# Optimization experiments

Hardware: AMD Instinct MI355X
Metric: run time of the kernel (lower is better)

Reference implementation:

```python
import jax, jax.numpy as jnp
import numpy as np

N = 50000      # nodes
E = 600000     # edges
DIN = 128      # dim_in
DOUT = 128     # dim_out (mulhead=1)
DG = 64        # dim_gate


def setup_inputs() -> dict:
    key = jax.random.key(0)
    ks = jax.random.split(key, 10)
    rows = jax.random.randint(ks[0], (E,), 0, N, dtype=jnp.int32)   # dest nodes
    cols = jax.random.randint(ks[1], (E,), 0, N, dtype=jnp.int32)   # src nodes
    vals = jax.random.uniform(ks[2], (E,), dtype=jnp.float32)       # adj_norm values
    feat = jax.random.normal(ks[3], (N, DIN), dtype=jnp.float32)
    s = 1.0 / np.sqrt(DIN)
    W0 = jax.random.normal(ks[4], (DIN, DOUT), dtype=jnp.float32) * s
    b0 = jnp.zeros((DOUT,), dtype=jnp.float32)
    W1 = jax.random.normal(ks[5], (DIN, DOUT), dtype=jnp.float32) * s
    b1 = jnp.zeros((DOUT,), dtype=jnp.float32)
    att = jax.random.normal(ks[6], (2 * DOUT,), dtype=jnp.float32) * 0.1  # attention param [1, 2*DOUT] flattened
    W_pool = jax.random.normal(ks[7], (DIN, DG), dtype=jnp.float32) * s    # weight_pool_gate
    W_gate = jax.random.normal(ks[8], (2 * DIN + DG, 1), dtype=jnp.float32) * 0.05  # weight_gate, mulhead=1
    offset0 = jnp.zeros((DOUT,), dtype=jnp.float32)
    scale0 = jnp.ones((DOUT,), dtype=jnp.float32)
    offset1 = jnp.zeros((DOUT,), dtype=jnp.float32)
    scale1 = jnp.ones((DOUT,), dtype=jnp.float32)
    return dict(rows=rows, cols=cols, vals=vals, feat=feat, W0=W0, b0=b0,
                W1=W1, b1=b1, att=att, W_pool=W_pool, W_gate=W_gate,
                offset0=offset0, scale0=scale0, offset1=offset1, scale1=scale1)


def _batch_norm(x, scale, offset):
    # per-node norm over the feature dim (unbiased=False), matching _batch_norm
    m = x.mean(axis=1, keepdims=True)
    v = x.var(axis=1, keepdims=True) + 1e-9
    return (x - m) * scale * jax.lax.rsqrt(v) + offset


def reference(rows, cols, vals, feat, W0, b0, W1, b1, att, W_pool, W_gate,
              offset0, scale0, offset1, scale1):
    n = feat.shape[0]
    d = W0.shape[1]
    # --- gate value (GaAN eq. 3) ---
    zj = feat @ W_pool                                   # [N, DG]
    neigh_zj = jax.ops.segment_max(zj[cols], rows, num_segments=n)  # per-row max over neighbors
    neigh_zj = jnp.where(jnp.isfinite(neigh_zj), neigh_zj, 0.0)     # empty rows -> zeros
    neigh_mean = jax.ops.segment_sum(vals[:, None] * feat[cols], rows, num_segments=n)  # spmm(adj, feat)
    gate = jnp.concatenate([feat, neigh_zj, neigh_mean], axis=1) @ W_gate  # [N, 1]
    # --- per-order feature transforms (order=1, mulhead=1) ---
    h0 = jax.nn.relu(feat @ W0 + b0)                     # order 0 (self)
    h1 = jax.nn.relu(feat @ W1 + b1)                     # order 1 (neighbor)
    # --- sparse attention aggregation ---
    a_self = jax.nn.leaky_relu(h0 @ att[:d], 0.2)        # [N]
    a_neigh = jax.nn.leaky_relu(h1 @ att[d:], 0.2)       # [N]
    e = a_self[rows] + a_neigh[cols]                     # per-edge score (replaces adj values)
    agg = jax.ops.segment_sum(e[:, None] * h1[cols], rows, num_segments=n)  # spmm(att_adj, h1)
    agg = agg * gate[:, :1]                              # gated
    # --- per-node batch norm, then 'mean' aggregation (sum of orders) ---
    return _batch_norm(h0, scale0, offset0) + _batch_norm(agg, scale1, offset1)
```

## Files before the change

kernel.cpp:

```cpp
#include <hip/hip_runtime.h>

#define DIN 128
#define DG 64

static __device__ __forceinline__ unsigned short f2bf(float x) {
    unsigned u = __builtin_bit_cast(unsigned, x);
    u = (u + 0x7FFF + ((u >> 16) & 1)) >> 16;
    return (unsigned short)u;
}
static __device__ __forceinline__ float bf2f(unsigned short s) {
    return __builtin_bit_cast(float, (unsigned)s << 16);
}

__global__ void k_deg(const int* __restrict__ rows, int* __restrict__ deg,
                      int* __restrict__ slot, int E) {
    int e = blockIdx.x * blockDim.x + threadIdx.x;
    if (e < E) slot[e] = atomicAdd(&deg[rows[e]], 1);
}

__global__ __launch_bounds__(1024) void k_scan1(const int* __restrict__ deg,
                                                int* __restrict__ rowptr,
                                                int* __restrict__ bsum, int n) {
    __shared__ int wsum[16];
    __shared__ int woff[16];
    int tid = threadIdx.x;
    int lane = tid & 63, w = tid >> 6;
    int i = blockIdx.x * 1024 + tid;
    int v = (i < n) ? deg[i] : 0;
    int x = v;
    #pragma unroll
    for (int off = 1; off < 64; off <<= 1) {
        int y = __shfl_up(x, off, 64);
        if (lane >= off) x += y;
    }
    if (lane == 63) wsum[w] = x;
    __syncthreads();
    if (w == 0) {
        int t = (lane < 16) ? wsum[lane] : 0;
        int xx = t;
        #pragma unroll
        for (int off = 1; off < 16; off <<= 1) {
            int y = __shfl_up(xx, off, 64);
            if (lane >= off) xx += y;
        }
        if (lane < 16) woff[lane] = xx - t;
    }
    __syncthreads();
    if (i < n) rowptr[i] = x - v + woff[w];
    if (tid == 1023) bsum[blockIdx.x] = woff[15] + wsum[15];
}

__global__ void k_scan2(const int* __restrict__ bsum, int* __restrict__ boff,
                        int* __restrict__ rowptr, int nb, int n) {
    int lane = threadIdx.x;
    int v = (lane < nb) ? bsum[lane] : 0;
    int x = v;
    #pragma unroll
    for (int off = 1; off < 64; off <<= 1) {
        int y = __shfl_up(x, off, 64);
        if (lane >= off) x += y;
    }
    boff[lane] = x - v;
    if (lane == 63) rowptr[n] = x;
}

__global__ void k_scan3(int* __restrict__ rowptr, const int* __restrict__ boff, int n) {
    int i = blockIdx.x * blockDim.x + threadIdx.x;
    if (i < n) rowptr[i] += boff[i >> 10];
}

__global__ void k_scatter(const int* __restrict__ rows, const int* __restrict__ cols,
                          const float* __restrict__ vals,
                          const int* __restrict__ rowptr, const int* __restrict__ slot,
                          int2* __restrict__ cv, int E) {
    int e = blockIdx.x * blockDim.x + threadIdx.x;
    if (e < E) {
        int dst = rowptr[rows[e]] + slot[e];
        cv[dst] = make_int2(cols[e], __builtin_bit_cast(int, vals[e]));
    }
}

__global__ void k_edgemeta(const int2* __restrict__ cv,
                           const float* __restrict__ a_neigh,
                           const float* __restrict__ fdotg,
                           float4* __restrict__ meta, int E) {
    int j = blockIdx.x * blockDim.x + threadIdx.x;
    if (j < E) {
        int2 p = cv[j];
        int c = p.x;
        float val = __builtin_bit_cast(float, p.y);
        meta[j] = make_float4(__builtin_bit_cast(float, c),
                              a_neigh[c], val * fdotg[c], 0.f);
    }
}

#define AS_LD 132
template<int TN, int TTN, int MODE>
static __device__ __forceinline__ void gemm_body(
    const float* __restrict__ feat, const float* __restrict__ B,
    const float* __restrict__ bias,
    const float* __restrict__ att, const float* __restrict__ Wg,
    float* __restrict__ h0, unsigned short* __restrict__ hb, float* __restrict__ zj,
    float* __restrict__ a_self, float* __restrict__ a_neigh,
    float* __restrict__ gpart, float* __restrict__ fdotg,
    int N, float* As, float* Bs) {
    int tid = threadIdx.x;
    int tx = tid & 15, ty = tid >> 4;
    int m0 = blockIdx.x * 128;
    float acc[8][TTN];
    #pragma unroll
    for (int r = 0; r < 8; ++r)
        #pragma unroll
        for (int c = 0; c < TTN; ++c) acc[r][c] = 0.f;
    float gdot[8], fdot[8];
    #pragma unroll
    for (int r = 0; r < 8; ++r) { gdot[r] = 0.f; fdot[r] = 0.f; }

    for (int kc = 0; kc < 128; kc += 32) {
        for (int i = tid; i < 1024; i += 256) {
            int m = i >> 3, kq = (i & 7) << 2;
            int node = m0 + m;
            float4 f;
            if (node < N) f = *(const float4*)&feat[(size_t)node * 128 + kc + kq];
            else          f = make_float4(0.f, 0.f, 0.f, 0.f);
            As[(kq + 0) * AS_LD + m] = f.x;
            As[(kq + 1) * AS_LD + m] = f.y;
            As[(kq + 2) * AS_LD + m] = f.z;
            As[(kq + 3) * AS_LD + m] = f.w;
        }
        for (int i = tid; i < 8 * TN; i += 256) {
            int k = i / (TN / 4), cq = (i % (TN / 4)) << 2;
            *(float4*)&Bs[k * TN + cq] = *(const float4*)&B[(size_t)(kc + k) * TN + cq];
        }
        __syncthreads();
        #pragma unroll 8
        for (int kk = 0; kk < 32; ++kk) {
            const float* ar = &As[kk * AS_LD];
            float4 a0 = *(const float4*)(ar + 4 * tx);
            float4 a1 = *(const float4*)(ar + 64 + 4 * tx);
            const float* br = &Bs[kk * TN + TTN * ty];
            float4 b0v = *(const float4*)br;
            float a[8] = {a0.x, a0.y, a0.z, a0.w, a1.x, a1.y, a1.z, a1.w};
            float b[TTN];
            b[0] = b0v.x; b[1] = b0v.y; b[2] = b0v.z; b[3] = b0v.w;
            if (TTN == 8) {
                float4 b1v = *(const float4*)(br + 4);
                b[4] = b1v.x; b[5] = b1v.y; b[6] = b1v.z; b[7] = b1v.w;
            }
            #pragma unroll
            for (int r = 0; r < 8; ++r)
                #pragma unroll
                for (int c = 0; c < TTN; ++c) acc[r][c] += a[r] * b[c];
            if (MODE == 0) {
                float g1 = Wg[kc + kk];
                float g2 = Wg[192 + kc + kk];
                #pragma unroll
                for (int r = 0; r < 8; ++r) {
                    gdot[r] += a[r] * g1;
                    fdot[r] += a[r] * g2;
                }
            }
        }
        __syncthreads();
    }
    float bb[TTN];
    #pragma unroll
    for (int c = 0; c < TTN; ++c) bb[c] = (MODE == 2) ? 0.f : bias[TTN * ty + c];
    float attv[TTN];
    if (MODE <= 1) {
        #pragma unroll
        for (int c = 0; c < TTN; ++c) attv[c] = att[(MODE == 0 ? 0 : 128) + TTN * ty + c];
    }
    float* red = Bs;
    #pragma unroll
    for (int r = 0; r < 8; ++r) {
        int ridx = (r < 4) ? (4 * tx + r) : (64 + 4 * tx + (r - 4));
        int node = m0 + ridx;
        float v[TTN];
        #pragma unroll
        for (int c = 0; c < TTN; ++c) {
            v[c] = acc[r][c] + bb[c];
            if (MODE != 2) v[c] = fmaxf(v[c], 0.f);
        }
        if (MODE <= 1) {
            float pa = 0.f;
            #pragma unroll
            for (int c = 0; c < TTN; ++c) pa += v[c] * attv[c];
            red[ty * 128 + ridx] = pa;
        }
        if (node < N) {
            if (MODE == 0) {
                #pragma unroll
                for (int g = 0; g < TTN / 4; ++g)
                    *(float4*)&h0[(size_t)node * 128 + TTN * ty + g * 4] =
                        make_float4(v[g*4], v[g*4+1], v[g*4+2], v[g*4+3]);
            } else if (MODE == 1) {
                unsigned p[4];
                #pragma unroll
                for (int g = 0; g < 4; ++g)
                    p[g] = (unsigned)f2bf(v[2*g]) | ((unsigned)f2bf(v[2*g+1]) << 16);
                *(uint4*)&hb[(size_t)node * 128 + 8 * ty] = make_uint4(p[0], p[1], p[2], p[3]);
            } else {
                *(float4*)&zj[(size_t)node * 64 + 4 * ty] =
                    make_float4(v[0], v[1], v[2], v[3]);
            }
        }
    }
    if (MODE == 0 && ty == 0) {
        #pragma unroll
        for (int r = 0; r < 8; ++r) {
            int ridx = (r < 4) ? (4 * tx + r) : (64 + 4 * tx + (r - 4));
            int node = m0 + ridx;
            if (node < N) { gpart[node] = gdot[r]; fdotg[node] = fdot[r]; }
        }
    }
    if (MODE <= 1) {
        __syncthreads();
        if (tid < 128) {
            float s = 0.f;
            #pragma unroll
            for (int t = 0; t < 16; ++t) s += red[t * 128 + tid];
            int node = m0 + tid;
            if (node < N) {
                float av = (s >= 0.f) ? s : 0.2f * s;
                if (MODE == 0) a_self[node] = av;
                else           a_neigh[node] = av;
            }
        }
    }
}

__global__ __launch_bounds__(256) void k_gemm3(
    const float* __restrict__ feat,
    const float* __restrict__ W0, const float* __restrict__ b0,
    const float* __restrict__ W1, const float* __restrict__ b1,
    const float* __restrict__ Wp,
    const float* __restrict__ att, const float* __restrict__ Wg,
    float* __restrict__ h0, unsigned short* __restrict__ hb, float* __restrict__ zj,
    float* __restrict__ a_self, float* __restrict__ a_neigh,
    float* __restrict__ gpart, float* __restrict__ fdotg, int N) {
    __shared__ float As[32 * AS_LD];
    __shared__ float Bs[32 * 128];
    int g = blockIdx.y;
    if (g == 0)      gemm_body<128, 8, 0>(feat, W0, b0, att, Wg, h0, hb, zj, a_self, a_neigh, gpart, fdotg, N, As, Bs);
    else if (g == 1) gemm_body<128, 8, 1>(feat, W1, b1, att, Wg, h0, hb, zj, a_self, a_neigh, gpart, fdotg, N, As, Bs);
    else             gemm_body< 64, 4, 2>(feat, Wp, nullptr, att, Wg, h0, hb, zj, a_self, a_neigh, gpart, fdotg, N, As, Bs);
}

template<int C>
static __device__ __forceinline__ void agg_chunk(
    const float4* __restrict__ meta, int j, int lane, float asr,
    const unsigned short* __restrict__ hb, const float* __restrict__ zj,
    float2& acca, float& zmax, float& vfsum) {
    float4 m[C];
    #pragma unroll
    for (int t = 0; t < C; ++t) m[t] = meta[j + t];
    ushort2 hv[C]; float zv[C];
    #pragma unroll
    for (int t = 0; t < C; ++t) {
        int c = __builtin_bit_cast(int, m[t].x);
        hv[t] = ((const ushort2*)(hb + (size_t)c * 128))[lane];
        zv[t] = zj[(size_t)c * 64 + lane];
    }
    #pragma unroll
    for (int t = 0; t < C; ++t) {
        float es = asr + m[t].y;
        acca.x += es * bf2f(hv[t].x);
        acca.y += es * bf2f(hv[t].y);
        zmax = fmaxf(zmax, zv[t]);
        vfsum += m[t].z;
    }
}

__global__ __launch_bounds__(256) void k_aggregate(
    const float4* __restrict__ meta, const int* __restrict__ rowptr,
    const float* __restrict__ h0, const unsigned short* __restrict__ hb,
    const float* __restrict__ zj,
    const float* __restrict__ a_self, const float* __restrict__ gpart,
    const float* __restrict__ Wg,
    const float* __restrict__ scale0, const float* __restrict__ offset0,
    const float* __restrict__ scale1, const float* __restrict__ offset1,
    float* __restrict__ out, int N) {
    int r = blockIdx.x * 4 + (threadIdx.x >> 6);
    int lane = threadIdx.x & 63;
    if (r >= N) return;
    int jb = rowptr[r], je = rowptr[r + 1];
    float2 acca = {0.f, 0.f};
    float zmax = -__builtin_inff();
    float vfsum = 0.f;
    float asr = a_self[r];
    int j = jb;
    while (j + 8 <= je) { agg_chunk<8>(meta, j, lane, asr, hb, zj, acca, zmax, vfsum); j += 8; }
    if (j + 4 <= je)    { agg_chunk<4>(meta, j, lane, asr, hb, zj, acca, zmax, vfsum); j += 4; }
    while (j < je)      { agg_chunk<1>(meta, j, lane, asr, hb, zj, acca, zmax, vfsum); j += 1; }
    if (jb == je) zmax = 0.f;
    float gs = zmax * Wg[128 + lane];
    #pragma unroll
    for (int off = 32; off; off >>= 1) gs += __shfl_xor(gs, off, 64);
    float gate = gpart[r] + gs + vfsum;
    float2 ag = {acca.x * gate, acca.y * gate};
    float2 x0 = ((const float2*)(h0 + (size_t)r * 128))[lane];
    float m0s = x0.x + x0.y;
    #pragma unroll
    for (int off = 32; off; off >>= 1) m0s += __shfl_xor(m0s, off, 64);
    float m0 = m0s * (1.f / 128.f);
    float d0x = x0.x - m0, d0y = x0.y - m0;
    float v0s = d0x * d0x + d0y * d0y;
    #pragma unroll
    for (int off = 32; off; off >>= 1) v0s += __shfl_xor(v0s, off, 64);
    float inv0 = rsqrtf(v0s * (1.f / 128.f) + 1e-9f);
    float m1s = ag.x + ag.y;
    #pragma unroll
    for (int off = 32; off; off >>= 1) m1s += __shfl_xor(m1s, off, 64);
    float m1 = m1s * (1.f / 128.f);
    float d1x = ag.x - m1, d1y = ag.y - m1;
    float v1s = d1x * d1x + d1y * d1y;
    #pragma unroll
    for (int off = 32; off; off >>= 1) v1s += __shfl_xor(v1s, off, 64);
    float inv1 = rsqrtf(v1s * (1.f / 128.f) + 1e-9f);
    float2 sc0 = ((const float2*)scale0)[lane], of0 = ((const float2*)offset0)[lane];
    float2 sc1 = ((const float2*)scale1)[lane], of1 = ((const float2*)offset1)[lane];
    float2 o;
    o.x = d0x * sc0.x * inv0 + of0.x + d1x * sc1.x * inv1 + of1.x;
    o.y = d0y * sc0.y * inv0 + of0.y + d1y * sc1.y * inv1 + of1.y;
    ((float2*)(out + (size_t)r * 128))[lane] = o;
}

extern "C" void kernel_launch(void* const* d_in, const int* in_sizes, int n_in,
                              void* d_out, int out_size, void* d_ws, size_t ws_size,
                              hipStream_t stream) {
    const int*   rows   = (const int*)d_in[0];
    const int*   cols   = (const int*)d_in[1];
    const float* vals   = (const float*)d_in[2];
    const float* feat   = (const float*)d_in[3];
    const float* W0     = (const float*)d_in[4];
    const float* b0     = (const float*)d_in[5];
    const float* W1     = (const float*)d_in[6];
    const float* b1     = (const float*)d_in[7];
    const float* att    = (const float*)d_in[8];
    const float* Wp     = (const float*)d_in[9];
    const float* Wg     = (const float*)d_in[10];
    const float* offset0 = (const float*)d_in[11];
    const float* scale0  = (const float*)d_in[12];
    const float* offset1 = (const float*)d_in[13];
    const float* scale1  = (const float*)d_in[14];
    float* out = (float*)d_out;

    const int E = in_sizes[0];
    const int N = in_sizes[3] / DIN;

    char* ws = (char*)d_ws;
    float* h0          = (float*)ws;          ws += (size_t)N * 128 * sizeof(float);
    unsigned short* hb = (unsigned short*)ws; ws += (size_t)N * 128 * sizeof(unsigned short);
    float* zj          = (float*)ws;          ws += (size_t)N * 64 * sizeof(float);
    float* a_self  = (float*)ws; ws += (size_t)N * sizeof(float);
    float* a_neigh = (float*)ws; ws += (size_t)N * sizeof(float);
    float* gpart   = (float*)ws; ws += (size_t)N * sizeof(float);
    float* fdotg   = (float*)ws; ws += (size_t)N * sizeof(float);
    int* deg      = (int*)ws; ws += (size_t)(N + 1) * sizeof(int);
    int* rowptr   = (int*)ws; ws += (size_t)(N + 1) * sizeof(int);
    int* bsum     = (int*)ws; ws += 64 * sizeof(int);
    int* boff     = (int*)ws; ws += 64 * sizeof(int);
    int* slot     = (int*)ws; ws += (size_t)E * sizeof(int);
    int2* cv      = (int2*)ws; ws += (size_t)E * sizeof(int2);
    ws = (char*)(((size_t)ws + 15) & ~(size_t)15);
    float4* meta  = (float4*)ws; ws += (size_t)E * sizeof(float4);

    hipMemsetAsync(deg, 0, (size_t)(N + 1) * sizeof(int), stream);

    k_deg<<<(E + 255) / 256, 256, 0, stream>>>(rows, deg, slot, E);
    int nb = (N + 1023) >> 10;
    k_scan1<<<nb, 1024, 0, stream>>>(deg, rowptr, bsum, N);
    k_scan2<<<1, 64, 0, stream>>>(bsum, boff, rowptr, nb, N);
    k_scan3<<<(N + 255) / 256, 256, 0, stream>>>(rowptr, boff, N);
    k_scatter<<<(E + 255) / 256, 256, 0, stream>>>(rows, cols, vals, rowptr, slot, cv, E);

    int mt = (N + 127) / 128;
    dim3 gg(mt, 3);
    k_gemm3<<<gg, 256, 0, stream>>>(feat, W0, b0, W1, b1, Wp, att, Wg,
                                    h0, hb, zj, a_self, a_neigh, gpart, fdotg, N);

    k_edgemeta<<<(E + 255) / 256, 256, 0, stream>>>(cv, a_neigh, fdotg, meta, E);

    int nb4 = (N + 3) / 4;
    k_aggregate<<<nb4, 256, 0, stream>>>(meta, rowptr, h0, hb, zj,
                                         a_self, gpart, Wg,
                                         scale0, offset0, scale1, offset1, out, N);
}
```

Baseline: 278.2 us.

## Move W0/W1 GEMMs to bf16 MFMA and fuse scatter with edge metadata

Replaces the fp32 FMA GEMM for the W0 and W1 transforms with a bf16 MFMA kernel. A new prep kernel converts feat to bf16 and computes the gate dot products, and a tiny kernel transposes the weights into bf16. The Wpool GEMM stays fp32 in its own kernel. The separate scatter and edge-metadata passes are merged into one kernel that writes meta directly, which drops the cv intermediate array. This cuts GEMM compute time and one pass over the edges, at the cost of bf16 precision in h0 and extra launches plus a feat conversion pass.

Result: no change. 280.8 us (+1.0%).

```diff
diff --git a/kernel.cpp b/kernel.cpp
--- a/kernel.cpp
+++ b/kernel.cpp
@@ -2,6 +2,9 @@
 
 #define DIN 128
 #define DG 64
+
+typedef __attribute__((ext_vector_type(8))) short short8;
+typedef __attribute__((ext_vector_type(4))) float f32x4;
 
 static __device__ __forceinline__ unsigned short f2bf(float x) {
     unsigned u = __builtin_bit_cast(unsigned, x);
@@ -69,53 +72,143 @@
     if (i < n) rowptr[i] += boff[i >> 10];
 }
 
-__global__ void k_scatter(const int* __restrict__ rows, const int* __restrict__ cols,
-                          const float* __restrict__ vals,
-                          const int* __restrict__ rowptr, const int* __restrict__ slot,
-                          int2* __restrict__ cv, int E) {
-    int e = blockIdx.x * blockDim.x + threadIdx.x;
-    if (e < E) {
-        int dst = rowptr[rows[e]] + slot[e];
-        cv[dst] = make_int2(cols[e], __builtin_bit_cast(int, vals[e]));
-    }
-}
-
-__global__ void k_edgemeta(const int2* __restrict__ cv,
-                           const float* __restrict__ a_neigh,
-                           const float* __restrict__ fdotg,
-                           float4* __restrict__ meta, int E) {
-    int j = blockIdx.x * blockDim.x + threadIdx.x;
-    if (j < E) {
-        int2 p = cv[j];
-        int c = p.x;
-        float val = __builtin_bit_cast(float, p.y);
-        meta[j] = make_float4(__builtin_bit_cast(float, c),
-                              a_neigh[c], val * fdotg[c], 0.f);
+__global__ __launch_bounds__(256) void k_prep(
+    const float* __restrict__ feat, const float* __restrict__ Wg,
+    unsigned short* __restrict__ featb,
+    float* __restrict__ gpart, float* __restrict__ fdotg, int N, int Npad) {
+    int r = blockIdx.x * 4 + (threadIdx.x >> 6);
+    int lane = threadIdx.x & 63;
+    if (r >= Npad) return;
+    if (r >= N) {
+        ((ushort2*)(featb + (size_t)r * 128))[lane] = make_ushort2(0, 0);
+        return;
+    }
+    float2 f = ((const float2*)(feat + (size_t)r * 128))[lane];
+    ((ushort2*)(featb + (size_t)r * 128))[lane] = make_ushort2(f2bf(f.x), f2bf(f.y));
+    float2 G  = ((const float2*)Wg)[lane];
+    float2 G2 = ((const float2*)(Wg + 192))[lane];
+    float s2 = f.x * G.x + f.y * G.y;
+    float s3 = f.x * G2.x + f.y * G2.y;
+    #pragma unroll
+    for (int off = 32; off; off >>= 1) {
+        s2 += __shfl_xor(s2, off, 64);
+        s3 += __shfl_xor(s3, off, 64);
+    }
+    if (lane == 0) { gpart[r] = s2; fdotg[r] = s3; }
+}
+
+__global__ __launch_bounds__(256) void k_wt(
+    const float* __restrict__ W0, const float* __restrict__ W1,
+    unsigned short* __restrict__ Bt) {
+    int c = threadIdx.x;
+    const float* W = (c < 128) ? W0 : W1;
+    int cc = c & 127;
+    for (int k = 0; k < 128; ++k)
+        Bt[c * 128 + k] = f2bf(W[k * 128 + cc]);
+}
+
+#define ALD 136
+__global__ __launch_bounds__(256) void k_gemm_mfma(
+    const unsigned short* __restrict__ featb, const unsigned short* __restrict__ Bt,
+    const float* __restrict__ b0, const float* __restrict__ b1,
+    const float* __restrict__ att,
+    float* __restrict__ h0, unsigned short* __restrict__ hb,
+    float* __restrict__ a_self, float* __restrict__ a_neigh, int N) {
+    __shared__ unsigned short As[64 * ALD];
+    __shared__ float sredA[128], nredA[128];
+    int tid = threadIdx.x;
+    int m0 = blockIdx.x * 64;
+    for (int i = tid; i < 1024; i += 256) {
+        int row = i >> 4, ch = i & 15;
+        uint4 v = *(const uint4*)&featb[(size_t)(m0 + row) * 128 + ch * 8];
+        *(uint4*)&As[row * ALD + ch * 8] = v;
+    }
+    __syncthreads();
+    int w = tid >> 6, lane = tid & 63;
+    int lm = lane & 15, q = lane >> 4;
+    f32x4 acc[4][4];
+    #pragma unroll
+    for (int rt = 0; rt < 4; ++rt)
+        #pragma unroll
+        for (int ct = 0; ct < 4; ++ct)
+            #pragma unroll
+            for (int r = 0; r < 4; ++r) acc[rt][ct][r] = 0.f;
+    #pragma unroll
+    for (int ks = 0; ks < 4; ++ks) {
+        short8 a[4], b[4];
+        #pragma unroll
+        for (int rt = 0; rt < 4; ++rt)
+            a[rt] = *(const short8*)&As[(rt * 16 + lm) * ALD + ks * 32 + q * 8];
+        #pragma unroll
+        for (int ct = 0; ct < 4; ++ct)
+            b[ct] = *(const short8*)&Bt[(size_t)(w * 64 + ct * 16 + lm) * 128 + ks * 32 + q * 8];
+        #pragma unroll
+        for (int rt = 0; rt < 4; ++rt)
+            #pragma unroll
+            for (int ct = 0; ct < 4; ++ct)
+                acc[rt][ct] = __builtin_amdgcn_mfma_f32_16x16x32_bf16(a[rt], b[ct], acc[rt][ct], 0, 0, 0);
+    }
+    float sacc[4][4];
+    #pragma unroll
+    for (int rt = 0; rt < 4; ++rt)
+        #pragma unroll
+        for (int r = 0; r < 4; ++r) sacc[rt][r] = 0.f;
+    #pragma unroll
+    for (int ct = 0; ct < 4; ++ct) {
+        int col = w * 64 + ct * 16 + lm;
+        float attc = att[col];
+        float bias = (w < 2) ? b0[col] : b1[col - 128];
+        #pragma unroll
+        for (int rt = 0; rt < 4; ++rt) {
+            #pragma unroll
+            for (int r = 0; r < 4; ++r) {
+                float v = acc[rt][ct][r] + bias;
+                v = fmaxf(v, 0.f);
+                sacc[rt][r] += v * attc;
+                int node = m0 + rt * 16 + q * 4 + r;
+                if (node < N) {
+                    if (w < 2) h0[(size_t)node * 128 + col] = v;
+                    else       hb[(size_t)node * 128 + (col - 128)] = f2bf(v);
+                }
+            }
+        }
+    }
+    float* red = (w < 2) ? sredA : nredA;
+    #pragma unroll
+    for (int rt = 0; rt < 4; ++rt)
+        #pragma unroll
+        for (int r = 0; r < 4; ++r) {
+            float s = sacc[rt][r];
+            s += __shfl_xor(s, 1, 64); s += __shfl_xor(s, 2, 64);
+            s += __shfl_xor(s, 4, 64); s += __shfl_xor(s, 8, 64);
+            if (lm == 0) red[(w & 1) * 64 + rt * 16 + q * 4 + r] = s;
+        }
+    __syncthreads();
+    if (tid < 64) {
+        int node = m0 + tid;
+        if (node < N) {
+            float s  = sredA[tid] + sredA[64 + tid];
+            float nn = nredA[tid] + nredA[64 + tid];
+            a_self[node]  = (s  >= 0.f) ? s  : 0.2f * s;
+            a_neigh[node] = (nn >= 0.f) ? nn : 0.2f * nn;
+        }
     }
 }
 
 #define AS_LD 132
-template<int TN, int TTN, int MODE>
-static __device__ __forceinline__ void gemm_body(
-    const float* __restrict__ feat, const float* __restrict__ B,
-    const float* __restrict__ bias,
-    const float* __restrict__ att, const float* __restrict__ Wg,
-    float* __restrict__ h0, unsigned short* __restrict__ hb, float* __restrict__ zj,
-    float* __restrict__ a_self, float* __restrict__ a_neigh,
-    float* __restrict__ gpart, float* __restrict__ fdotg,
-    int N, float* As, float* Bs) {
+__global__ __launch_bounds__(256) void k_gemm_zj(
+    const float* __restrict__ feat, const float* __restrict__ Wp,
+    float* __restrict__ zj, int N) {
+    __shared__ float As[32 * AS_LD];
+    __shared__ float Bs[32 * 64];
     int tid = threadIdx.x;
     int tx = tid & 15, ty = tid >> 4;
     int m0 = blockIdx.x * 128;
-    float acc[8][TTN];
+    float acc[8][4];
     #pragma unroll
     for (int r = 0; r < 8; ++r)
         #pragma unroll
-        for (int c = 0; c < TTN; ++c) acc[r][c] = 0.f;
-    float gdot[8], fdot[8];
-    #pragma unroll
-    for (int r = 0; r < 8; ++r) { gdot[r] = 0.f; fdot[r] = 0.f; }
-
+        for (int c = 0; c < 4; ++c) acc[r][c] = 0.f;
     for (int kc = 0; kc < 128; kc += 32) {
         for (int i = tid; i < 1024; i += 256) {
             int m = i >> 3, kq = (i & 7) << 2;
@@ -128,9 +221,9 @@
             As[(kq + 2) * AS_LD + m] = f.z;
             As[(kq + 3) * AS_LD + m] = f.w;
         }
-        for (int i = tid; i < 8 * TN; i += 256) {
-            int k = i / (TN / 4), cq = (i % (TN / 4)) << 2;
-            *(float4*)&Bs[k * TN + cq] = *(const float4*)&B[(size_t)(kc + k) * TN + cq];
+        for (int i = tid; i < 512; i += 256) {
+            int k = i >> 4, cq = (i & 15) << 2;
+            *(float4*)&Bs[k * 64 + cq] = *(const float4*)&Wp[(size_t)(kc + k) * 64 + cq];
         }
         __syncthreads();
         #pragma unroll 8
@@ -138,113 +231,37 @@
             const float* ar = &As[kk * AS_LD];
             float4 a0 = *(const float4*)(ar + 4 * tx);
             float4 a1 = *(const float4*)(ar + 64 + 4 * tx);
-            const float* br = &Bs[kk * TN + TTN * ty];
-            float4 b0v = *(const float4*)br;
+            float4 b0v = *(const float4*)&Bs[kk * 64 + 4 * ty];
             float a[8] = {a0.x, a0.y, a0.z, a0.w, a1.x, a1.y, a1.z, a1.w};
-            float b[TTN];
-            b[0] = b0v.x; b[1] = b0v.y; b[2] = b0v.z; b[3] = b0v.w;
-            if (TTN == 8) {
-                float4 b1v = *(const float4*)(br + 4);
-                b[4] = b1v.x; b[5] = b1v.y; b[6] = b1v.z; b[7] = b1v.w;
+            #pragma unroll
+            for (int r = 0; r < 8; ++r) {
+                acc[r][0] += a[r] * b0v.x; acc[r][1] += a[r] * b0v.y;
+                acc[r][2] += a[r] * b0v.z; acc[r][3] += a[r] * b0v.w;
             }
-            #pragma unroll
-            for (int r = 0; r < 8; ++r)
-                #pragma unroll
-                for (int c = 0; c < TTN; ++c) acc[r][c] += a[r] * b[c];
-            if (MODE == 0) {
-                float g1 = Wg[kc + kk];
-                float g2 = Wg[192 + kc + kk];
-                #pragma unroll
-                for (int r = 0; r < 8; ++r) {
-                    gdot[r] += a[r] * g1;
-                    fdot[r] += a[r] * g2;
-                }
-            }
         }
         __syncthreads();
     }
-    float bb[TTN];
-    #pragma unroll
-    for (int c = 0; c < TTN; ++c) bb[c] = (MODE == 2) ? 0.f : bias[TTN * ty + c];
-    float attv[TTN];
-    if (MODE <= 1) {
-        #pragma unroll
-        for (int c = 0; c < TTN; ++c) attv[c] = att[(MODE == 0 ? 0 : 128) + TTN * ty + c];
-    }
-    float* red = Bs;
     #pragma unroll
     for (int r = 0; r < 8; ++r) {
-        int ridx = (r < 4) ? (4 * tx + r) : (64 + 4 * tx + (r - 4));
-        int node = m0 + ridx;
-        float v[TTN];
-        #pragma unroll
-        for (int c = 0; c < TTN; ++c) {
-            v[c] = acc[r][c] + bb[c];
-            if (MODE != 2) v[c] = fmaxf(v[c], 0.f);
-        }
-        if (MODE <= 1) {
-            float pa = 0.f;
-            #pragma unroll
-            for (int c = 0; c < TTN; ++c) pa += v[c] * attv[c];
-            red[ty * 128 + ridx] = pa;
-        }
-        if (node < N) {
-            if (MODE == 0) {
-                #pragma unroll
-                for (int g = 0; g < TTN / 4; ++g)
-                    *(float4*)&h0[(size_t)node * 128 + TTN * ty + g * 4] =
-                        make_float4(v[g*4], v[g*4+1], v[g*4+2], v[g*4+3]);
-            } else if (MODE == 1) {
-                unsigned p[4];
-                #pragma unroll
-                for (int g = 0; g < 4; ++g)
-                    p[g] = (unsigned)f2bf(v[2*g]) | ((unsigned)f2bf(v[2*g+1]) << 16);
-                *(uint4*)&hb[(size_t)node * 128 + 8 * ty] = make_uint4(p[0], p[1], p[2], p[3]);
-            } else {
-                *(float4*)&zj[(size_t)node * 64 + 4 * ty] =
-                    make_float4(v[0], v[1], v[2], v[3]);
-            }
-        }
-    }
-    if (MODE == 0 && ty == 0) {
-        #pragma unroll
-        for (int r = 0; r < 8; ++r) {
-            int ridx = (r < 4) ? (4 * tx + r) : (64 + 4 * tx + (r - 4));
-            int node = m0 + ridx;
-            if (node < N) { gpart[node] = gdot[r]; fdotg[node] = fdot[r]; }
-        }
-    }
-    if (MODE <= 1) {
-        __syncthreads();
-        if (tid < 128) {
-            float s = 0.f;
-            #pragma unroll
-            for (int t = 0; t < 16; ++t) s += red[t * 128 + tid];
-            int node = m0 + tid;
-            if (node < N) {
-                float av = (s >= 0.f) ? s : 0.2f * s;
-                if (MODE == 0) a_self[node] = av;
-                else           a_neigh[node] = av;
-            }
-        }
-    }
-}
-
-__global__ __launch_bounds__(256) void k_gemm3(
-    const float* __restrict__ feat,
-    const float* __restrict__ W0, const float* __restrict__ b0,
-    const float* __restrict__ W1, const float* __restrict__ b1,
-    const float* __restrict__ Wp,
-    const float* __restrict__ att, const float* __restrict__ Wg,
-    float* __restrict__ h0, unsigned short* __restrict__ hb, float* __restrict__ zj,
-    float* __restrict__ a_self, float* __restrict__ a_neigh,
-    float* __restrict__ gpart, float* __restrict__ fdotg, int N) {
-    __shared__ float As[32 * AS_LD];
-    __shared__ float Bs[32 * 128];
-    int g = blockIdx.y;
-    if (g == 0)      gemm_body<128, 8, 0>(feat, W0, b0, att, Wg, h0, hb, zj, a_self, a_neigh, gpart, fdotg, N, As, Bs);
-    else if (g == 1) gemm_body<128, 8, 1>(feat, W1, b1, att, Wg, h0, hb, zj, a_self, a_neigh, gpart, fdotg, N, As, Bs);
-    else             gemm_body< 64, 4, 2>(feat, Wp, nullptr, att, Wg, h0, hb, zj, a_self, a_neigh, gpart, fdotg, N, As, Bs);
+        int node = m0 + ((r < 4) ? (4 * tx + r) : (64 + 4 * tx + (r - 4)));
+        if (node >= N) continue;
+        *(float4*)&zj[(size_t)node * 64 + 4 * ty] =
+            make_float4(acc[r][0], acc[r][1], acc[r][2], acc[r][3]);
+    }
+}
+
+__global__ void k_scatter_meta(const int* __restrict__ rows, const int* __restrict__ cols,
+                               const float* __restrict__ vals,
+                               const int* __restrict__ rowptr, const int* __restrict__ slot,
+                               const float* __restrict__ a_neigh, const float* __restrict__ fdotg,
+                               float4* __restrict__ meta, int E) {
+    int e = blockIdx.x * blockDim.x + threadIdx.x;
+    if (e < E) {
+        int c = cols[e];
+        int dst = rowptr[rows[e]] + slot[e];
+        meta[dst] = make_float4(__builtin_bit_cast(float, c),
+                                a_neigh[c], vals[e] * fdotg[c], 0.f);
+    }
 }
 
 template<int C>
@@ -348,11 +365,14 @@
 
     const int E = in_sizes[0];
     const int N = in_sizes[3] / DIN;
+    const int Npad = (N + 63) & ~63;
 
     char* ws = (char*)d_ws;
-    float* h0          = (float*)ws;          ws += (size_t)N * 128 * sizeof(float);
-    unsigned short* hb = (unsigned short*)ws; ws += (size_t)N * 128 * sizeof(unsigned short);
-    float* zj          = (float*)ws;          ws += (size_t)N * 64 * sizeof(float);
+    float* h0            = (float*)ws;          ws += (size_t)N * 128 * sizeof(float);
+    unsigned short* hb   = (unsigned short*)ws; ws += (size_t)N * 128 * sizeof(unsigned short);
+    float* zj            = (float*)ws;          ws += (size_t)N * 64 * sizeof(float);
+    unsigned short* featb = (unsigned short*)ws; ws += (size_t)Npad * 128 * sizeof(unsigned short);
+    unsigned short* Bt   = (unsigned short*)ws; ws += (size_t)256 * 128 * sizeof(unsigned short);
     float* a_self  = (float*)ws; ws += (size_t)N * sizeof(float);
     float* a_neigh = (float*)ws; ws += (size_t)N * sizeof(float);
     float* gpart   = (float*)ws; ws += (size_t)N * sizeof(float);
@@ -362,7 +382,6 @@
     int* bsum     = (int*)ws; ws += 64 * sizeof(int);
     int* boff     = (int*)ws; ws += 64 * sizeof(int);
     int* slot     = (int*)ws; ws += (size_t)E * sizeof(int);
-    int2* cv      = (int2*)ws; ws += (size_t)E * sizeof(int2);
     ws = (char*)(((size_t)ws + 15) & ~(size_t)15);
     float4* meta  = (float4*)ws; ws += (size_t)E * sizeof(float4);
 
@@ -373,14 +392,16 @@
     k_scan1<<<nb, 1024, 0, stream>>>(deg, rowptr, bsum, N);
     k_scan2<<<1, 64, 0, stream>>>(bsum, boff, rowptr, nb, N);
     k_scan3<<<(N + 255) / 256, 256, 0, stream>>>(rowptr, boff, N);
-    k_scatter<<<(E + 255) / 256, 256, 0, stream>>>(rows, cols, vals, rowptr, slot, cv, E);
-
-    int mt = (N + 127) / 128;
-    dim3 gg(mt, 3);
-    k_gemm3<<<gg, 256, 0, stream>>>(feat, W0, b0, W1, b1, Wp, att, Wg,
-                                    h0, hb, zj, a_self, a_neigh, gpart, fdotg, N);
-
-    k_edgemeta<<<(E + 255) / 256, 256, 0, stream>>>(cv, a_neigh, fdotg, meta, E);
+
+    k_prep<<<Npad / 4, 256, 0, stream>>>(feat, Wg, featb, gpart, fdotg, N, Npad);
+    k_wt<<<1, 256, 0, stream>>>(W0, W1, Bt);
+
+    k_gemm_zj<<<(N + 127) / 128, 256, 0, stream>>>(feat, Wp, zj, N);
+    k_gemm_mfma<<<Npad / 64, 256, 0, stream>>>(featb, Bt, b0, b1, att,
+                                               h0, hb, a_self, a_neigh, N);
+
+    k_scatter_meta<<<(E + 255) / 256, 256, 0, stream>>>(rows, cols, vals, rowptr, slot,
+                                                        a_neigh, fdotg, meta, E);
 
     int nb4 = (N + 3) / 4;
     k_aggregate<<<nb4, 256, 0, stream>>>(meta, rowptr, h0, hb, zj,
```
